# Kernel optimization log

Measured on AMD Instinct MI355X. Metric: run time of the kernel, lower is better.

Reference implementation:

```python
import jax, jax.numpy as jnp
import numpy as np

HEADS = 4
DIM_HEAD = 32  # total inner dim; per-head dim = DIM_HEAD // HEADS = 8
SCALE = DIM_HEAD ** -0.5  # faithful to original: scale uses dim_head, not per-head dim


def setup_inputs() -> dict:
    key = jax.random.key(0)
    k_x, k_q, k_kv, k_o, k_pe = jax.random.split(key, 5)
    B, L, dim = 131072, 4, 256
    inner = DIM_HEAD
    x = jax.random.normal(k_x, (B, L, dim), dtype=jnp.float32)
    Wq = jax.random.normal(k_q, (dim, inner), dtype=jnp.float32) * 0.02
    Wkv = jax.random.normal(k_kv, (dim, 2 * inner), dtype=jnp.float32) * 0.02
    Wo = jax.random.normal(k_o, (inner, dim), dtype=jnp.float32) * 0.02
    bo = jnp.zeros((dim,), dtype=jnp.float32)
    pos_emb = jax.random.normal(k_pe, (1, HEADS, L, L), dtype=jnp.float32)
    return {"x": x, "Wq": Wq, "Wkv": Wkv, "Wo": Wo, "bo": bo, "pos_emb": pos_emb}


def reference(x, Wq, Wkv, Wo, bo, pos_emb):
    B, L, dim = x.shape
    dh = DIM_HEAD // HEADS  # per-head dim
    q = x @ Wq                       # [B, L, inner]
    kv = x @ Wkv                     # [B, L, 2*inner]
    k, v = jnp.split(kv, 2, axis=-1)
    # [B, L, inner] -> [B, heads, L, dh]
    split_heads = lambda t: t.reshape(B, L, HEADS, dh).transpose(0, 2, 1, 3)
    q, k, v = map(split_heads, (q, k, v))
    q = q * SCALE
    sim = jnp.einsum('bhid,bhjd->bhij', q, k) + pos_emb  # [B, heads, L, L]
    attn = jax.nn.softmax(sim, axis=-1)
    out = jnp.einsum('bhij,bhjd->bhid', attn, v)         # [B, heads, L, dh]
    out = out.transpose(0, 2, 1, 3).reshape(B, L, HEADS * dh)
    return out @ Wo + bo             # [B, L, dim]
```

## Files before the change

kernel.cpp:

```cpp
#include <hip/hip_runtime.h>
#include <hip/hip_bf16.h>

typedef float  f32x4  __attribute__((ext_vector_type(4)));
typedef __bf16 bf16x8 __attribute__((ext_vector_type(8)));

#define SCALE_QK 0.17677669529663687f


template<int CTRL>
__device__ __forceinline__ float dpp_add(float x) {
  int xi = __builtin_bit_cast(int, x);
  int yi = __builtin_amdgcn_mov_dpp(xi, CTRL, 0xF, 0xF, true);
  return x + __builtin_bit_cast(float, yi);
}

__global__ void pack_weights(const float* __restrict__ Wq, const float* __restrict__ Wkv,
                             const float* __restrict__ Wo, __bf16* __restrict__ wsf) {
  const int item = blockIdx.x * 256 + threadIdx.x;
  const int f = item >> 6, lane = item & 63;
  const int g = lane >> 4, c = lane & 15;
  union { bf16x8 v; __bf16 h[8]; } vv;
  if (f < 48) {
    const int kt = f / 6, ct = f - kt * 6;
    const int n = ct * 16 + c;
    #pragma unroll
    for (int j = 0; j < 8; ++j) {
      const int k = kt * 32 + g * 8 + j;
      vv.h[j] = (__bf16)((n < 32) ? Wq[k * 32 + n] : Wkv[k * 64 + (n - 32)]);
    }
  } else {
    const int ct = f - 48;
    const int n = ct * 16 + c;
    #pragma unroll
    for (int j = 0; j < 8; ++j) vv.h[j] = (__bf16)Wo[(g * 8 + j) * 256 + n];
  }
  *(bf16x8*)&wsf[item * 8] = vv.v;
}

#define MFMA(a, b, cc) __builtin_amdgcn_mfma_f32_16x16x32_bf16((a), (b), (cc), 0, 0, 0)
#define VMW(n) do { asm volatile("s_waitcnt vmcnt(" #n ")" ::: "memory"); \
                    __builtin_amdgcn_sched_barrier(0); } while (0)
#define WF(f) (((f) < 25) ? wfr[(f) % 25] \
                          : (*(const bf16x8*)&wfragL[(((f) < 25) ? 0 : (f) - 25) * 512 + lane * 8]))

#define LDS_TOTAL 163072

__global__ __launch_bounds__(256, 1) void fused_stattn(
    const float* __restrict__ x, const __bf16* __restrict__ wsf,
    const float* __restrict__ bo, const float* __restrict__ pe,
    float* __restrict__ out) {
  extern __shared__ char smem[];

  const int tid  = threadIdx.x;
  const int lane = tid & 63;
  const int wv   = tid >> 6;
  const int g    = lane >> 4;
  const int c    = lane & 15;

  __bf16* wfragL = (__bf16*)smem;
  char*   stg0   = smem + 23552 + wv * 33280;
  __bf16* aoW    = (__bf16*)(smem + 156672 + wv * 1280);
  float*  bo_l   = (float*)(smem + 161792);
  float*  pe_l   = (float*)(smem + 162816);

  bf16x8 wo[16];
  #pragma unroll
  for (int i = 0; i < 16; ++i)
    wo[i] = *(const bf16x8*)&wsf[((48 + i) * 64 + lane) * 8];
  bf16x8 wfr[25];
  #pragma unroll
  for (int i = 0; i < 25; ++i)
    wfr[i] = *(const bf16x8*)&wsf[(i * 64 + lane) * 8];

  #pragma unroll
  for (int it = 0; it < 6; ++it) {
    const int idx = it * 256 + tid;
    if (idx < 1472)
      *(bf16x8*)&wfragL[idx * 8] = *(const bf16x8*)&wsf[(1600 + idx) * 8];
  }
  bo_l[tid] = bo[tid];
  if (tid < 64) pe_l[tid] = pe[tid];

  #pragma unroll
  for (int i = 0; i < 16; ++i) asm volatile("" :: "v"(wo[i]));
  #pragma unroll
  for (int i = 0; i < 25; ++i) asm volatile("" :: "v"(wfr[i]));
  __syncthreads();

  const unsigned stg_lds = (unsigned)(unsigned long long)(void*)stg0;

  auto stage_tile = [&](unsigned dbase, int tile) {
    const float* src = x + (size_t)tile * 4096 + (lane << 2);
    #pragma unroll
    for (int r = 0; r < 16; ++r) {
      __builtin_amdgcn_global_load_lds(
          (const __attribute__((address_space(1))) void*)(src + r * 256),
          (__attribute__((address_space(3))) void*)(unsigned long long)(dbase + r * 1040),
          16, 0, 0);
    }
  };

  const int slot  = blockIdx.x * 4 + wv;
  const int tile0 = slot * 8;

  int cur = 0;
  stage_tile(stg_lds, tile0);

  for (int t = 0; t < 8; ++t) {
    const int tile = tile0 + t;
    asm volatile("s_waitcnt lgkmcnt(0)" ::: "memory");
    if (t < 7) stage_tile(stg_lds + (unsigned)((cur ^ 1) * 16640), tile + 1);
    VMW(16);

    char* stg = stg0 + cur * 16640;

    f32x4 acc0 = {0,0,0,0}, acc1 = {0,0,0,0}, acc2 = {0,0,0,0};
    f32x4 acc3 = {0,0,0,0}, acc4 = {0,0,0,0}, acc5 = {0,0,0,0};
    #pragma unroll
    for (int kt = 0; kt < 8; ++kt) {
      const f32x4 va = *(const f32x4*)(stg + c * 1040 + kt * 128 + g * 32);
      const f32x4 vb = *(const f32x4*)(stg + c * 1040 + kt * 128 + g * 32 + 16);
      union { bf16x8 v; __bf16 h[8]; } af;
      #pragma unroll
      for (int j = 0; j < 4; ++j) { af.h[j] = (__bf16)va[j]; af.h[4+j] = (__bf16)vb[j]; }
      acc0 = MFMA(af.v, WF(kt*6+0), acc0);
      acc1 = MFMA(af.v, WF(kt*6+1), acc1);
      acc2 = MFMA(af.v, WF(kt*6+2), acc2);
      acc3 = MFMA(af.v, WF(kt*6+3), acc3);
      acc4 = MFMA(af.v, WF(kt*6+4), acc4);
      acc5 = MFMA(af.v, WF(kt*6+5), acc5);
    }

    const int h0 = c >> 3;
    float ao0[4], ao1[4];
    #pragma unroll
    for (int p = 0; p < 2; ++p) {
      const f32x4 qa = p ? acc1 : acc0;
      const f32x4 ka = p ? acc3 : acc2;
      const f32x4 va = p ? acc5 : acc4;
      const int ph = 2 * p + h0;
      float sim[4][4];
      #pragma unroll
      for (int i = 0; i < 4; ++i)
        #pragma unroll
        for (int j = 0; j < 4; ++j) {
          float pr = qa[i] * ka[j];
          pr = dpp_add<0xB1>(pr);
          pr = dpp_add<0x4E>(pr);
          pr = dpp_add<0x141>(pr);
          sim[i][j] = pr * SCALE_QK + pe_l[ph * 16 + i * 4 + j];
        }
      #pragma unroll
      for (int i = 0; i < 4; ++i) {
        const float m = fmaxf(fmaxf(sim[i][0], sim[i][1]), fmaxf(sim[i][2], sim[i][3]));
        const float e0 = __expf(sim[i][0] - m), e1 = __expf(sim[i][1] - m);
        const float e2 = __expf(sim[i][2] - m), e3 = __expf(sim[i][3] - m);
        const float rs = 1.0f / (e0 + e1 + e2 + e3);
        const float o  = (e0*va[0] + e1*va[1] + e2*va[2] + e3*va[3]) * rs;
        if (p) ao1[i] = o; else ao0[i] = o;
      }
    }

    #pragma unroll
    for (int i = 0; i < 4; ++i) {
      aoW[(g*4 + i) * 40 + c]      = (__bf16)ao0[i];
      aoW[(g*4 + i) * 40 + 16 + c] = (__bf16)ao1[i];
    }
    const bf16x8 a2 = *(const bf16x8*)&aoW[c * 40 + g * 8];

    #pragma unroll
    for (int ct = 0; ct < 16; ++ct) {
      const f32x4 bv = *(const f32x4*)&bo_l[ct * 16 + g * 4];
      f32x4 o = MFMA(wo[ct], a2, bv);
      *(f32x4*)(stg + c * 1040 + ct * 64 + g * 16) = o;
    }

    {
      float* orow = out + (size_t)tile * 4096 + (lane << 2);
      #pragma unroll
      for (int r = 0; r < 16; ++r) {
        const f32x4 v = *(const f32x4*)(stg + r * 1040 + lane * 16);
        *(f32x4*)(orow + r * 256) = v;
      }
    }

    cur ^= 1;
  }
}

extern "C" void kernel_launch(void* const* d_in, const int* in_sizes, int n_in,
                              void* d_out, int out_size, void* d_ws, size_t ws_size,
                              hipStream_t stream) {
  const float* x   = (const float*)d_in[0];
  const float* Wq  = (const float*)d_in[1];
  const float* Wkv = (const float*)d_in[2];
  const float* Wo  = (const float*)d_in[3];
  const float* bo  = (const float*)d_in[4];
  const float* pe  = (const float*)d_in[5];
  float* out = (float*)d_out;
  __bf16* wsf = (__bf16*)d_ws;

  (void)hipFuncSetAttribute(reinterpret_cast<const void*>(fused_stattn),
                            hipFuncAttributeMaxDynamicSharedMemorySize, LDS_TOTAL);
  hipLaunchKernelGGL(pack_weights, dim3(16), dim3(256), 0, stream, Wq, Wkv, Wo, wsf);
  hipLaunchKernelGGL(fused_stattn, dim3(1024), dim3(256), LDS_TOTAL, stream,
                     x, wsf, bo, pe, out);
}
```

Baseline: 241.9 us.

## Hold weight fragments in AGPRs instead of VGPRs and LDS

Moves 60 of the 64 packed bf16 weight fragments (the QKV weights and most of Wo) into accumulation registers via inline v_accvgpr_write, then reads each back with v_accvgpr_read right before its MFMA. The QKV and Wo GEMMs no longer fetch weights from LDS; only the last four Wo fragments stay there. This shrinks the LDS footprint and LDS read traffic, but adds many accvgpr read instructions per tile and raises register pressure. It relies on inline asm register constraints, which the compiler may handle poorly, and includes a leftover redefined macro.

```diff
diff --git a/kernel.cpp b/kernel.cpp
--- a/kernel.cpp
+++ b/kernel.cpp
@@ -40,10 +40,34 @@
 #define MFMA(a, b, cc) __builtin_amdgcn_mfma_f32_16x16x32_bf16((a), (b), (cc), 0, 0, 0)
 #define VMW(n) do { asm volatile("s_waitcnt vmcnt(" #n ")" ::: "memory"); \
                     __builtin_amdgcn_sched_barrier(0); } while (0)
-#define WF(f) (((f) < 25) ? wfr[(f) % 25] \
-                          : (*(const bf16x8*)&wfragL[(((f) < 25) ? 0 : (f) - 25) * 512 + lane * 8]))
-
-#define LDS_TOTAL 163072
+
+#define AGPR_WR(dst, srcv) do {                                           \
+  union { bf16x8 v; int i[4]; } _u; _u.v = (srcv);                        \
+  asm volatile("v_accvgpr_write_b32 %0, %1" : "=a"((dst)[0]) : "v"(_u.i[0])); \
+  asm volatile("v_accvgpr_write_b32 %0, %1" : "=a"((dst)[1]) : "v"(_u.i[1])); \
+  asm volatile("v_accvgpr_write_b32 %0, %1" : "=a"((dst)[2]) : "v"(_u.i[2])); \
+  asm volatile("v_accvgpr_read_b32 %1, %1\n\t.purgem dummy" :: "X"(0), "X"(0)); \
+} while (0)
+
+#define AGPR_RD(dstv, src) do {                                           \
+  union { int i[4]; bf16x8 v; } _u;                                       \
+  asm volatile("v_accvgpr_read_b32 %0, %1" : "=v"(_u.i[0]) : "a"((src)[0])); \
+  asm volatile("v_accvgpr_read_b32 %0, %1" : "=v"(_u.i[1]) : "a"((src)[1])); \
+  asm volatile("v_accvgpr_read_b32 %0, %1" : "=v"(_u.i[2]) : "a"((src)[2])); \
+  asm volatile("v_accvgpr_read_b32 %0, %1" : "=v"(_u.i[3]) : "a"((src)[3])); \
+  dstv = _u.v;                                                            \
+} while (0)
+
+#undef AGPR_WR
+#define AGPR_WR(dst, srcv) do {                                           \
+  union { bf16x8 v; int i[4]; } _u; _u.v = (srcv);                        \
+  asm volatile("v_accvgpr_write_b32 %0, %1" : "=a"((dst)[0]) : "v"(_u.i[0])); \
+  asm volatile("v_accvgpr_write_b32 %0, %1" : "=a"((dst)[1]) : "v"(_u.i[1])); \
+  asm volatile("v_accvgpr_write_b32 %0, %1" : "=a"((dst)[2]) : "v"(_u.i[2])); \
+  asm volatile("v_accvgpr_write_b32 %0, %1" : "=a"((dst)[3]) : "v"(_u.i[3])); \
+} while (0)
+
+#define LDS_TOTAL 143616
 
 __global__ __launch_bounds__(256, 1) void fused_stattn(
     const float* __restrict__ x, const __bf16* __restrict__ wsf,
@@ -58,33 +82,24 @@
   const int c    = lane & 15;
 
   __bf16* wfragL = (__bf16*)smem;
-  char*   stg0   = smem + 23552 + wv * 33280;
-  __bf16* aoW    = (__bf16*)(smem + 156672 + wv * 1280);
-  float*  bo_l   = (float*)(smem + 161792);
-  float*  pe_l   = (float*)(smem + 162816);
-
-  bf16x8 wo[16];
+  char*   stg0   = smem + 4096 + wv * 33280;
+  __bf16* aoW    = (__bf16*)(smem + 137216 + wv * 1280);
+  float*  bo_l   = (float*)(smem + 142336);
+  float*  pe_l   = (float*)(smem + 143360);
+
+  int wA[60][4];
   #pragma unroll
-  for (int i = 0; i < 16; ++i)
-    wo[i] = *(const bf16x8*)&wsf[((48 + i) * 64 + lane) * 8];
-  bf16x8 wfr[25];
-  #pragma unroll
-  for (int i = 0; i < 25; ++i)
-    wfr[i] = *(const bf16x8*)&wsf[(i * 64 + lane) * 8];
-
-  #pragma unroll
-  for (int it = 0; it < 6; ++it) {
-    const int idx = it * 256 + tid;
-    if (idx < 1472)
-      *(bf16x8*)&wfragL[idx * 8] = *(const bf16x8*)&wsf[(1600 + idx) * 8];
+  for (int f = 0; f < 60; ++f) {
+    const bf16x8 w = *(const bf16x8*)&wsf[(f * 64 + lane) * 8];
+    AGPR_WR(wA[f], w);
+  }
+
+  {
+    const int idx = tid;
+    *(bf16x8*)&wfragL[idx * 8] = *(const bf16x8*)&wsf[(60 * 64 * 8 + idx * 8)];
   }
   bo_l[tid] = bo[tid];
   if (tid < 64) pe_l[tid] = pe[tid];
-
-  #pragma unroll
-  for (int i = 0; i < 16; ++i) asm volatile("" :: "v"(wo[i]));
-  #pragma unroll
-  for (int i = 0; i < 25; ++i) asm volatile("" :: "v"(wfr[i]));
   __syncthreads();
 
   const unsigned stg_lds = (unsigned)(unsigned long long)(void*)stg0;
@@ -123,12 +138,19 @@
       union { bf16x8 v; __bf16 h[8]; } af;
       #pragma unroll
       for (int j = 0; j < 4; ++j) { af.h[j] = (__bf16)va[j]; af.h[4+j] = (__bf16)vb[j]; }
-      acc0 = MFMA(af.v, WF(kt*6+0), acc0);
-      acc1 = MFMA(af.v, WF(kt*6+1), acc1);
-      acc2 = MFMA(af.v, WF(kt*6+2), acc2);
-      acc3 = MFMA(af.v, WF(kt*6+3), acc3);
-      acc4 = MFMA(af.v, WF(kt*6+4), acc4);
-      acc5 = MFMA(af.v, WF(kt*6+5), acc5);
+      bf16x8 b0, b1, b2, b3, b4, b5;
+      AGPR_RD(b0, wA[kt*6+0]);
+      AGPR_RD(b1, wA[kt*6+1]);
+      AGPR_RD(b2, wA[kt*6+2]);
+      AGPR_RD(b3, wA[kt*6+3]);
+      AGPR_RD(b4, wA[kt*6+4]);
+      AGPR_RD(b5, wA[kt*6+5]);
+      acc0 = MFMA(af.v, b0, acc0);
+      acc1 = MFMA(af.v, b1, acc1);
+      acc2 = MFMA(af.v, b2, acc2);
+      acc3 = MFMA(af.v, b3, acc3);
+      acc4 = MFMA(af.v, b4, acc4);
+      acc5 = MFMA(af.v, b5, acc5);
     }
 
     const int h0 = c >> 3;
@@ -171,7 +193,10 @@
     #pragma unroll
     for (int ct = 0; ct < 16; ++ct) {
       const f32x4 bv = *(const f32x4*)&bo_l[ct * 16 + g * 4];
-      f32x4 o = MFMA(wo[ct], a2, bv);
+      bf16x8 wb;
+      if (ct < 12) { AGPR_RD(wb, wA[48 + ct]); }
+      else         { wb = *(const bf16x8*)&wfragL[((ct - 12) * 64 + lane) * 8]; }
+      f32x4 o = MFMA(wb, a2, bv);
       *(f32x4*)(stg + c * 1040 + ct * 64 + g * 16) = o;
     }
 
```

After: 280.8 us. +16.1%, slower.
